# Kernel optimization log

Hardware: AMD Instinct MI355X
Metric: run time of the kernel (lower is better)

Reference implementation:

```python
import jax, jax.numpy as jnp
import numpy as np

VOL_RANGE = (-40.0, -40.0, -1.0, 40.0, 40.0, 5.4)
VOXEL = 0.8
SCENE = tuple(int((VOL_RANGE[i + 3] - VOL_RANGE[i]) / VOXEL) for i in range(3))  # (100, 100, 8)
B, G, F = 1, 128, 16


def _make_grid():
    # generate_grid(scene_shape, offset=0.5) * voxel_size + vol_range[:3]
    axes = [(jnp.arange(s, dtype=jnp.float32) + 0.5) * VOXEL + VOL_RANGE[i]
            for i, s in enumerate(SCENE)]
    gx, gy, gz = jnp.meshgrid(*axes, indexing='ij')
    return jnp.stack([gx, gy, gz], axis=-1).reshape(-1, 3)  # (N, 3)


def setup_inputs() -> dict:
    key = jax.random.key(0)
    k1, k2, k3, k4 = jax.random.split(key, 4)
    lo = jnp.array(VOL_RANGE[:3], dtype=jnp.float32)
    hi = jnp.array(VOL_RANGE[3:], dtype=jnp.float32)
    means3d = lo + jax.random.uniform(k1, (B, G, 3), dtype=jnp.float32) * (hi - lo)
    opacities = jax.random.uniform(k2, (B, G, 1), dtype=jnp.float32)
    features = jax.random.normal(k3, (B, G, F), dtype=jnp.float32)
    A = jax.random.normal(k4, (B, G, 3, 3), dtype=jnp.float32)
    covariances = jnp.einsum('bgij,bgkj->bgik', A, A) + 0.1 * jnp.eye(3, dtype=jnp.float32)
    return {
        'grid_coords': _make_grid(),
        'means3d': means3d,
        'opacities': opacities,
        'features': features,
        'covariances': covariances,
    }


def _splat_into_3d(grid_coords, means3d, opacities, covariances, features):
    # grid_coords: (N,3); means3d: (B,G,3); opacities: (B,G,1);
    # covariances: (B,G,3,3); features: (B,G,F)
    b, g, _ = means3d.shape
    n = grid_coords.shape[0]
    f = features.shape[-1]
    dtype = means3d.dtype

    def step(carry, xs):
        dens, feats, cnts = carry                 # (B,N,1), (B,N,F), (B,N,1)
        mean, opac, cov, feat = xs                # (B,3), (B,1), (B,3,3), (B,F)
        diff = grid_coords[None] - mean[:, None]  # (B,N,3)
        cov_inv = jnp.linalg.inv(cov)             # (B,3,3)
        maha = jnp.einsum('bni,bij,bnj->bn', diff, cov_inv, diff)[..., None]  # (B,N,1)
        mask = (maha <= 4.0).astype(dtype)        # (B,N,1)
        cnts = cnts + mask
        denom = jnp.maximum(cnts, 1e-6)
        w = jnp.exp(-0.5 * maha)                  # (B,N,1)
        d_g = opac[:, None] * w                   # (B,N,1)
        dens = dens + mask * (d_g - dens) / denom
        f_g = (opac * feat)[:, None] * w          # (B,N,F)
        feats = feats + mask * (f_g - feats) / denom
        return (dens, feats, cnts), None

    init = (jnp.zeros((b, n, 1), dtype),
            jnp.zeros((b, n, f), dtype),
            jnp.zeros((b, n, 1), dtype))
    xs = (jnp.swapaxes(means3d, 0, 1),
          jnp.swapaxes(opacities, 0, 1),
          jnp.swapaxes(covariances, 0, 1),
          jnp.swapaxes(features, 0, 1))
    (dens, feats, _), _ = jax.lax.scan(step, init, xs)
    return dens, feats


def reference(grid_coords, means3d, opacities, features, covariances):
    dens, feats = _splat_into_3d(grid_coords, means3d, opacities, covariances, features)
    b = dens.shape[0]
    dens = dens.reshape(b, *SCENE, 1)
    feats = feats.reshape(b, *SCENE, feats.shape[-1])
    return dens, feats
```

## Files before the change

### kernel.cpp

```cpp
#include <hip/hip_runtime.h>
#include <hip/hip_bf16.h>


#define GV_GMAX 128
#define GV_F 16
#define GV_NV 64
#define GV_NW 4
#define GV_RW (GV_F + 2)

__global__ __launch_bounds__(256)
void GaussianVoxelizer_40467181863368_kernel(
    const float* __restrict__ grid,
    const float* __restrict__ means,
    const float* __restrict__ opac,
    const float* __restrict__ feats,
    const float* __restrict__ covs,
    float* __restrict__ out_dens,
    float* __restrict__ out_feat,
    int N, int G)
{
    __shared__ float s_mean[GV_GMAX][3];
    __shared__ float s_op[GV_GMAX];
    __shared__ float s_inv[GV_GMAX][6];
    __shared__ float s_feat[GV_GMAX][GV_F];
    __shared__ float s_red[GV_NW][GV_NV][GV_RW];

    const int t = threadIdx.x;

    for (int g = t; g < G; g += blockDim.x) {
        const float c00 = covs[g * 9 + 0];
        const float c01 = covs[g * 9 + 1];
        const float c02 = covs[g * 9 + 2];
        const float c11 = covs[g * 9 + 4];
        const float c12 = covs[g * 9 + 5];
        const float c22 = covs[g * 9 + 8];
        const float m00 = c11 * c22 - c12 * c12;
        const float m01 = c02 * c12 - c01 * c22;
        const float m02 = c01 * c12 - c02 * c11;
        const float det = c00 * m00 + c01 * m01 + c02 * m02;
        const float rdet = 1.0f / det;
        s_inv[g][0] = m00 * rdet;
        s_inv[g][1] = m01 * rdet;
        s_inv[g][2] = m02 * rdet;
        s_inv[g][3] = (c00 * c22 - c02 * c02) * rdet;
        s_inv[g][4] = (c01 * c02 - c00 * c12) * rdet;
        s_inv[g][5] = (c00 * c11 - c01 * c01) * rdet;

        s_mean[g][0] = means[g * 3 + 0];
        s_mean[g][1] = means[g * 3 + 1];
        s_mean[g][2] = means[g * 3 + 2];
        s_op[g] = opac[g];
        #pragma unroll
        for (int f = 0; f < GV_F; ++f) s_feat[g][f] = feats[g * GV_F + f];
    }
    __syncthreads();

    const int wave = t >> 6;
    const int lane = t & 63;
    const int n = blockIdx.x * GV_NV + lane;

    float px = 0.0f, py = 0.0f, pz = 0.0f;
    if (n < N) {
        px = grid[n * 3 + 0];
        py = grid[n * 3 + 1];
        pz = grid[n * 3 + 2];
    }

    const int chunk = (G + GV_NW - 1) / GV_NW;
    const int g0 = wave * chunk;
    const int g1 = (g0 + chunk < G) ? (g0 + chunk) : G;

    float cnt = 0.0f;
    float sum_d = 0.0f;
    float sum_f[GV_F];
    #pragma unroll
    for (int f = 0; f < GV_F; ++f) sum_f[f] = 0.0f;

    if (n < N) {
        #pragma unroll 4
        for (int g = g0; g < g1; ++g) {
            const float dx = px - s_mean[g][0];
            const float dy = py - s_mean[g][1];
            const float dz = pz - s_mean[g][2];
            const float maha =
                s_inv[g][0] * dx * dx + s_inv[g][3] * dy * dy + s_inv[g][5] * dz * dz +
                2.0f * (s_inv[g][1] * dx * dy + s_inv[g][2] * dx * dz + s_inv[g][4] * dy * dz);
            if (maha <= 4.0f) {
                const float w = __expf(-0.5f * maha) * s_op[g];
                cnt += 1.0f;
                sum_d += w;
                #pragma unroll
                for (int f = 0; f < GV_F; ++f) sum_f[f] += w * s_feat[g][f];
            }
        }
    }

    {
        float* r = &s_red[wave][lane][0];
        r[0] = cnt;
        r[1] = sum_d;
        #pragma unroll
        for (int f = 0; f < GV_F; ++f) r[2 + f] = sum_f[f];
    }
    __syncthreads();

    if (t < GV_NV) {
        const int n2 = blockIdx.x * GV_NV + t;
        if (n2 < N) {
            float c = 0.0f, d = 0.0f;
            float ff[GV_F];
            #pragma unroll
            for (int f = 0; f < GV_F; ++f) ff[f] = 0.0f;
            #pragma unroll
            for (int w = 0; w < GV_NW; ++w) {
                const float* r = &s_red[w][t][0];
                c += r[0];
                d += r[1];
                #pragma unroll
                for (int f = 0; f < GV_F; ++f) ff[f] += r[2 + f];
            }
            const float inv_c = (c > 0.0f) ? (1.0f / c) : 0.0f;
            out_dens[n2] = d * inv_c;
            float4* fo = (float4*)(out_feat + (size_t)n2 * GV_F);
            #pragma unroll
            for (int q = 0; q < 4; ++q) {
                fo[q] = make_float4(ff[4 * q + 0] * inv_c,
                                    ff[4 * q + 1] * inv_c,
                                    ff[4 * q + 2] * inv_c,
                                    ff[4 * q + 3] * inv_c);
            }
        }
    }
}

extern "C" void kernel_launch(void* const* d_in, const int* in_sizes, int n_in,
                              void* d_out, int out_size, void* d_ws, size_t ws_size,
                              hipStream_t stream) {
    const float* grid  = (const float*)d_in[0];
    const float* means = (const float*)d_in[1];
    const float* opac  = (const float*)d_in[2];
    const float* feats = (const float*)d_in[3];
    const float* covs  = (const float*)d_in[4];

    const int N = in_sizes[0] / 3;
    const int G = in_sizes[2];

    float* out_dens = (float*)d_out;
    float* out_feat = (float*)d_out + N;

    const int block = 256;
    const int grid_n = (N + GV_NV - 1) / GV_NV;
    GaussianVoxelizer_40467181863368_kernel<<<grid_n, block, 0, stream>>>(
        grid, means, opac, feats, covs, out_dens, out_feat, N, G);
}
```

Baseline: 71.44 us.

## Precompute scaled inverse covariances in a prep kernel and read params from global

Moves the per-Gaussian covariance inversion and parameter packing into a separate small prep kernel that writes packed float4 records to workspace. The main kernel drops its per-block shared-memory staging and barrier, and reads uniform float4 parameters straight from global memory. The quadratic form is folded to include the -0.5 factor and the symmetric 2x terms, and opacity is pre-multiplied into features, so the exponent and threshold test need fewer operations. It adds a second kernel launch, and parameter loads now go through cache instead of LDS.

Result: slower. 79.99 us (+12.0%).

```diff
diff --git a/kernel.cpp b/kernel.cpp
--- a/kernel.cpp
+++ b/kernel.cpp
@@ -2,59 +2,66 @@
 #include <hip/hip_bf16.h>
 
 
-#define GV_GMAX 128
 #define GV_F 16
 #define GV_NV 64
 #define GV_NW 4
 #define GV_RW (GV_F + 2)
+#define GV_Q 7
+
+__global__ __launch_bounds__(128)
+void gv_prep(const float* __restrict__ means,
+             const float* __restrict__ opac,
+             const float* __restrict__ feats,
+             const float* __restrict__ covs,
+             float4* __restrict__ P,
+             int G)
+{
+    const int g = blockIdx.x * blockDim.x + threadIdx.x;
+    if (g >= G) return;
+
+    const float c00 = covs[g * 9 + 0];
+    const float c01 = covs[g * 9 + 1];
+    const float c02 = covs[g * 9 + 2];
+    const float c11 = covs[g * 9 + 4];
+    const float c12 = covs[g * 9 + 5];
+    const float c22 = covs[g * 9 + 8];
+    const float m00 = c11 * c22 - c12 * c12;
+    const float m01 = c02 * c12 - c01 * c22;
+    const float m02 = c01 * c12 - c02 * c11;
+    const float det = c00 * m00 + c01 * m01 + c02 * m02;
+    const float s = -0.5f / det;
+    const float k00 = m00 * s;
+    const float k01 = m01 * (2.0f * s);
+    const float k02 = m02 * (2.0f * s);
+    const float k11 = (c00 * c22 - c02 * c02) * s;
+    const float k12 = (c01 * c02 - c00 * c12) * (2.0f * s);
+    const float k22 = (c00 * c11 - c01 * c01) * s;
+
+    const float op = opac[g];
+    float4* q = P + (size_t)g * GV_Q;
+    q[0] = make_float4(means[g * 3 + 0], means[g * 3 + 1], means[g * 3 + 2], op);
+    q[1] = make_float4(k00, k01, k02, k11);
+    q[2] = make_float4(k12, k22, 0.0f, 0.0f);
+    #pragma unroll
+    for (int j = 0; j < 4; ++j) {
+        q[3 + j] = make_float4(op * feats[g * GV_F + 4 * j + 0],
+                               op * feats[g * GV_F + 4 * j + 1],
+                               op * feats[g * GV_F + 4 * j + 2],
+                               op * feats[g * GV_F + 4 * j + 3]);
+    }
+}
 
 __global__ __launch_bounds__(256)
 void GaussianVoxelizer_40467181863368_kernel(
     const float* __restrict__ grid,
-    const float* __restrict__ means,
-    const float* __restrict__ opac,
-    const float* __restrict__ feats,
-    const float* __restrict__ covs,
+    const float4* __restrict__ P,
     float* __restrict__ out_dens,
     float* __restrict__ out_feat,
     int N, int G)
 {
-    __shared__ float s_mean[GV_GMAX][3];
-    __shared__ float s_op[GV_GMAX];
-    __shared__ float s_inv[GV_GMAX][6];
-    __shared__ float s_feat[GV_GMAX][GV_F];
     __shared__ float s_red[GV_NW][GV_NV][GV_RW];
 
     const int t = threadIdx.x;
-
-    for (int g = t; g < G; g += blockDim.x) {
-        const float c00 = covs[g * 9 + 0];
-        const float c01 = covs[g * 9 + 1];
-        const float c02 = covs[g * 9 + 2];
-        const float c11 = covs[g * 9 + 4];
-        const float c12 = covs[g * 9 + 5];
-        const float c22 = covs[g * 9 + 8];
-        const float m00 = c11 * c22 - c12 * c12;
-        const float m01 = c02 * c12 - c01 * c22;
-        const float m02 = c01 * c12 - c02 * c11;
-        const float det = c00 * m00 + c01 * m01 + c02 * m02;
-        const float rdet = 1.0f / det;
-        s_inv[g][0] = m00 * rdet;
-        s_inv[g][1] = m01 * rdet;
-        s_inv[g][2] = m02 * rdet;
-        s_inv[g][3] = (c00 * c22 - c02 * c02) * rdet;
-        s_inv[g][4] = (c01 * c02 - c00 * c12) * rdet;
-        s_inv[g][5] = (c00 * c11 - c01 * c01) * rdet;
-
-        s_mean[g][0] = means[g * 3 + 0];
-        s_mean[g][1] = means[g * 3 + 1];
-        s_mean[g][2] = means[g * 3 + 2];
-        s_op[g] = opac[g];
-        #pragma unroll
-        for (int f = 0; f < GV_F; ++f) s_feat[g][f] = feats[g * GV_F + f];
-    }
-    __syncthreads();
-
     const int wave = t >> 6;
     const int lane = t & 63;
     const int n = blockIdx.x * GV_NV + lane;
@@ -79,18 +86,44 @@
     if (n < N) {
         #pragma unroll 4
         for (int g = g0; g < g1; ++g) {
-            const float dx = px - s_mean[g][0];
-            const float dy = py - s_mean[g][1];
-            const float dz = pz - s_mean[g][2];
-            const float maha =
-                s_inv[g][0] * dx * dx + s_inv[g][3] * dy * dy + s_inv[g][5] * dz * dz +
-                2.0f * (s_inv[g][1] * dx * dy + s_inv[g][2] * dx * dz + s_inv[g][4] * dy * dz);
-            if (maha <= 4.0f) {
-                const float w = __expf(-0.5f * maha) * s_op[g];
+            const float4 q0 = P[g * GV_Q + 0];
+            const float4 q1 = P[g * GV_Q + 1];
+            const float4 q2 = P[g * GV_Q + 2];
+            const float dx = px - q0.x;
+            const float dy = py - q0.y;
+            const float dz = pz - q0.z;
+            float a = q1.x * dx;
+            a = fmaf(q1.y, dy, a);
+            a = fmaf(q1.z, dz, a);
+            float tt = a * dx;
+            float b = q1.w * dy;
+            b = fmaf(q2.x, dz, b);
+            tt = fmaf(b, dy, tt);
+            tt = fmaf(q2.y * dz, dz, tt);
+            if (tt >= -2.0f) {
+                const float w = __expf(tt);
                 cnt += 1.0f;
-                sum_d += w;
-                #pragma unroll
-                for (int f = 0; f < GV_F; ++f) sum_f[f] += w * s_feat[g][f];
+                sum_d = fmaf(q0.w, w, sum_d);
+                const float4 f0 = P[g * GV_Q + 3];
+                const float4 f1 = P[g * GV_Q + 4];
+                const float4 f2 = P[g * GV_Q + 5];
+                const float4 f3 = P[g * GV_Q + 6];
+                sum_f[0]  = fmaf(f0.x, w, sum_f[0]);
+                sum_f[1]  = fmaf(f0.y, w, sum_f[1]);
+                sum_f[2]  = fmaf(f0.z, w, sum_f[2]);
+                sum_f[3]  = fmaf(f0.w, w, sum_f[3]);
+                sum_f[4]  = fmaf(f1.x, w, sum_f[4]);
+                sum_f[5]  = fmaf(f1.y, w, sum_f[5]);
+                sum_f[6]  = fmaf(f1.z, w, sum_f[6]);
+                sum_f[7]  = fmaf(f1.w, w, sum_f[7]);
+                sum_f[8]  = fmaf(f2.x, w, sum_f[8]);
+                sum_f[9]  = fmaf(f2.y, w, sum_f[9]);
+                sum_f[10] = fmaf(f2.z, w, sum_f[10]);
+                sum_f[11] = fmaf(f2.w, w, sum_f[11]);
+                sum_f[12] = fmaf(f3.x, w, sum_f[12]);
+                sum_f[13] = fmaf(f3.y, w, sum_f[13]);
+                sum_f[14] = fmaf(f3.z, w, sum_f[14]);
+                sum_f[15] = fmaf(f3.w, w, sum_f[15]);
             }
         }
     }
@@ -145,11 +178,15 @@
     const int N = in_sizes[0] / 3;
     const int G = in_sizes[2];
 
+    float4* P = (float4*)d_ws;
+
     float* out_dens = (float*)d_out;
     float* out_feat = (float*)d_out + N;
+
+    gv_prep<<<(G + 127) / 128, 128, 0, stream>>>(means, opac, feats, covs, P, G);
 
     const int block = 256;
     const int grid_n = (N + GV_NV - 1) / GV_NV;
     GaussianVoxelizer_40467181863368_kernel<<<grid_n, block, 0, stream>>>(
-        grid, means, opac, feats, covs, out_dens, out_feat, N, G);
+        grid, P, out_dens, out_feat, N, G);
 }
```
